# Performance work log

Hardware: AMD Instinct MI355X
Metric: run time of the kernel (lower is better)

## Reference

```python
import jax, jax.numpy as jnp
import numpy as np

GROUPS = 32
HEADS = 4
EPS_GN = 1e-5
EPS_DEN = 1e-6


def group_norm(x, gamma, beta):
    b, c, h, w = x.shape
    xg = x.reshape(b, GROUPS, (c // GROUPS) * h * w)
    mu = xg.mean(axis=-1, keepdims=True)
    var = xg.var(axis=-1, keepdims=True)
    xn = ((xg - mu) * jax.lax.rsqrt(var + EPS_GN)).reshape(b, c, h, w)
    return xn * gamma[None, :, None, None] + beta[None, :, None, None]


def setup_inputs() -> dict:
    key = jax.random.key(0)
    ks = jax.random.split(key, 4)
    b, c, h, w = 16, 256, 64, 64
    x = jax.random.normal(ks[0], (b, c, h, w), dtype=jnp.float32)
    gamma = jnp.ones((c,), jnp.float32)
    beta = jnp.zeros((c,), jnp.float32)
    w_qkv = jax.random.normal(ks[1], (3 * c, c), jnp.float32) * (1.0 / np.sqrt(c))
    b_qkv = jnp.zeros((3 * c,), jnp.float32)
    w_out = jax.random.normal(ks[2], (c, c), jnp.float32) * (1.0 / np.sqrt(c))
    b_out = jnp.zeros((c,), jnp.float32)
    return {"x": x, "gamma": gamma, "beta": beta, "w_qkv": w_qkv,
            "b_qkv": b_qkv, "w_out": w_out, "b_out": b_out}


def reference(x, gamma, beta, w_qkv, b_qkv, w_out, b_out):
    b, c, h, w = x.shape
    d = c // HEADS
    n = h * w
    xn = group_norm(x, gamma, beta)
    # 1x1 conv == channel GEMM: [b,3c,h,w]
    qkv = jnp.einsum('bchw,oc->bohw', xn, w_qkv) + b_qkv[None, :, None, None]
    q, k, v = jnp.split(qkv, 3, axis=1)
    # b (heads d) h w -> b heads d n
    q = q.reshape(b, HEADS, d, n)
    k = k.reshape(b, HEADS, d, n)
    v = v.reshape(b, HEADS, d, n)
    q = jax.nn.elu(q) + 1.0
    k = jax.nn.elu(k) + 1.0
    k_sum = k.sum(axis=-1)                                 # [b,H,d]
    kv = jnp.einsum('bhdn,bhen->bhde', k, v)               # [b,H,d,d]
    out = jnp.einsum('bhde,bhdn->bhen', kv, q)             # [b,H,d,n]
    denom = jnp.einsum('bhdn,bhd->bhn', q, k_sum)          # [b,H,n]
    out = out / (denom[:, :, None, :] + EPS_DEN)
    out = out.reshape(b, c, h, w)
    out = jnp.einsum('bchw,oc->bohw', out, w_out) + b_out[None, :, None, None]
    return out + x
```

## Files before the change

kernel.cpp:

```cpp
#include <hip/hip_runtime.h>
#include <stdint.h>

#define BATCH 16
#define CH    256
#define NSP   4096
#define NH    4
#define HD    64

typedef __attribute__((ext_vector_type(8))) short bf16x8;
typedef __attribute__((ext_vector_type(4))) float f32x4;
typedef __attribute__((ext_vector_type(4))) unsigned int u32x4;

__device__ __forceinline__ short f2bf(float f) {
    union { float f; unsigned u; } v; v.f = f;
    unsigned r = (v.u + 0x7fffu + ((v.u >> 16) & 1u)) >> 16;
    return (short)r;
}
__device__ __forceinline__ float bf2f(short s) {
    union { float f; unsigned u; } v; v.u = ((unsigned)(unsigned short)s) << 16;
    return v.f;
}

__global__ __launch_bounds__(256) void k_pre(
        const float* __restrict__ x, const float* __restrict__ wq, const float* __restrict__ wo,
        float* __restrict__ mu, float* __restrict__ rstd,
        short* __restrict__ wq_bf, short* __restrict__ wo_bf) {
    int bg = blockIdx.x;
    if (bg < 512) {
        const float4* p = (const float4*)(x + (size_t)bg * 32768);
        float s = 0.f, sq = 0.f;
        for (int i = threadIdx.x; i < 8192; i += 256) {
            float4 v = p[i];
            s  += v.x + v.y + v.z + v.w;
            sq += v.x * v.x + v.y * v.y + v.z * v.z + v.w * v.w;
        }
        for (int off = 32; off; off >>= 1) { s += __shfl_down(s, off); sq += __shfl_down(sq, off); }
        __shared__ float ls[4], lq[4];
        int w = threadIdx.x >> 6;
        if ((threadIdx.x & 63) == 0) { ls[w] = s; lq[w] = sq; }
        __syncthreads();
        if (threadIdx.x == 0) {
            float S = ls[0] + ls[1] + ls[2] + ls[3];
            float Q = lq[0] + lq[1] + lq[2] + lq[3];
            float m = S / 32768.f;
            float var = Q / 32768.f - m * m;
            mu[bg] = m; rstd[bg] = rsqrtf(var + 1e-5f);
        }
    } else {
        int idx = ((bg - 512) * 256 + threadIdx.x) * 4;
        float4 v;
        short* dst;
        if (idx < 196608) { v = *(const float4*)(wq + idx); dst = wq_bf + idx; }
        else              { v = *(const float4*)(wo + (idx - 196608)); dst = wo_bf + (idx - 196608); }
        unsigned p0 = ((unsigned)(unsigned short)f2bf(v.x)) | (((unsigned)(unsigned short)f2bf(v.y)) << 16);
        unsigned p1 = ((unsigned)(unsigned short)f2bf(v.z)) | (((unsigned)(unsigned short)f2bf(v.w)) << 16);
        uint2 pk; pk.x = p0; pk.y = p1;
        *(uint2*)dst = pk;
    }
}

__global__ __launch_bounds__(256) void k_gnqkv(
        const float* __restrict__ x, const float* __restrict__ gamma, const float* __restrict__ beta,
        const float* __restrict__ mu, const float* __restrict__ rstd,
        const short* __restrict__ wq_bf, const float* __restrict__ b_qkv,
        short* __restrict__ q_t, short* __restrict__ kvp_bf, float* __restrict__ ksp) {
    int b = blockIdx.y, nt = blockIdx.x;
    int n0 = nt * 64;
    __shared__ short Blds[64 * 264];
    __shared__ union UR {
        struct { short kst[64 * 72]; short vst[64 * 72]; } s;
        short cst[64 * 136];
    } R;
    int t = threadIdx.x, lane = t & 63, wv = t >> 6, lr = lane & 15, quad = lane >> 4;

    {
        const float* xb = x + (size_t)b * CH * NSP;
        int m = t & 15, cq = t >> 4;
        for (int cb = 0; cb < 16; cb++) {
            int c = cb * 16 + cq;
            int g = c >> 3;
            float sc = rstd[b * 32 + g] * gamma[c];
            float sh = beta[c] - mu[b * 32 + g] * sc;
            float4 v = *(const float4*)(xb + (size_t)c * NSP + n0 + m * 4);
            float vv[4] = {v.x, v.y, v.z, v.w};
            #pragma unroll
            for (int j = 0; j < 4; j++) {
                int n = m * 4 + j;
                int cc = c ^ (((n >> 4) & 3) << 3);
                Blds[n * 264 + cc] = f2bf(vv[j] * sc + sh);
            }
        }
    }
    __syncthreads();

    for (int h = 0; h < 4; h++) {
        int base_row = (wv < 2 ? 256 : 512) + h * 64;
        int sub = (wv & 1) * 32;
        f32x4 acc[2][4] = {};
        for (int k0 = 0; k0 < 256; k0 += 32) {
            bf16x8 afr[2], bfr[4];
            #pragma unroll
            for (int mi = 0; mi < 2; mi++)
                afr[mi] = *(const bf16x8*)(wq_bf + (size_t)(base_row + sub + mi * 16 + lr) * 256 + k0 + quad * 8);
            #pragma unroll
            for (int ni = 0; ni < 4; ni++) {
                int rr = ni * 16 + lr;
                bfr[ni] = *(const bf16x8*)(Blds + rr * 264 + ((k0 + quad * 8) ^ (((rr >> 4) & 3) << 3)));
            }
            #pragma unroll
            for (int mi = 0; mi < 2; mi++)
                #pragma unroll
                for (int ni = 0; ni < 4; ni++)
                    acc[mi][ni] = __builtin_amdgcn_mfma_f32_16x16x32_bf16(afr[mi], bfr[ni], acc[mi][ni], 0, 0, 0);
        }
        __syncthreads();
        short* dst = (wv < 2) ? R.s.kst : R.s.vst;
        bool is_k = (wv < 2);
        #pragma unroll
        for (int mi = 0; mi < 2; mi++)
          #pragma unroll
          for (int ni = 0; ni < 4; ni++)
            #pragma unroll
            for (int r = 0; r < 4; r++) {
                int ol = sub + mi * 16 + quad * 4 + r;
                int nl = ni * 16 + lr;
                float v = acc[mi][ni][r] + b_qkv[base_row + ol];
                if (is_k) v = v > 0.f ? v + 1.f : __expf(v);
                dst[ol * 72 + nl] = f2bf(v);
            }
        __syncthreads();
        {
            int d = t >> 2, nq = (t & 3) * 16;
            float s = 0.f;
            #pragma unroll
            for (int j = 0; j < 16; j++) s += bf2f(R.s.kst[d * 72 + nq + j]);
            s += __shfl_down(s, 2);
            s += __shfl_down(s, 1);
            if ((t & 3) == 0) ksp[((size_t)(b * 4 + h) * 64 + nt) * 64 + d] = s;
        }
        f32x4 acc2[4] = {};
        #pragma unroll
        for (int kk = 0; kk < 64; kk += 32) {
            bf16x8 af = *(const bf16x8*)(R.s.vst + (wv * 16 + lr) * 72 + kk + quad * 8);
            bf16x8 bfk[4];
            #pragma unroll
            for (int ni = 0; ni < 4; ni++)
                bfk[ni] = *(const bf16x8*)(R.s.kst + (ni * 16 + lr) * 72 + kk + quad * 8);
            #pragma unroll
            for (int ni = 0; ni < 4; ni++)
                acc2[ni] = __builtin_amdgcn_mfma_f32_16x16x32_bf16(af, bfk[ni], acc2[ni], 0, 0, 0);
        }
        short* kvdst = kvp_bf + ((size_t)(b * 4 + h) * 64 + nt) * 4096;
        #pragma unroll
        for (int ni = 0; ni < 4; ni++)
            #pragma unroll
            for (int r = 0; r < 4; r++)
                kvdst[(wv * 16 + quad * 4 + r) * 64 + ni * 16 + lr] = f2bf(acc2[ni][r]);
    }

    for (int mtq = 0; mtq < 2; mtq++) {
        f32x4 acc[2][4] = {};
        int wm = wv * 32;
        for (int k0 = 0; k0 < 256; k0 += 32) {
            bf16x8 afr[2], bfr[4];
            #pragma unroll
            for (int mi = 0; mi < 2; mi++)
                afr[mi] = *(const bf16x8*)(wq_bf + (size_t)(mtq * 128 + wm + mi * 16 + lr) * 256 + k0 + quad * 8);
            #pragma unroll
            for (int ni = 0; ni < 4; ni++) {
                int rr = ni * 16 + lr;
                bfr[ni] = *(const bf16x8*)(Blds + rr * 264 + ((k0 + quad * 8) ^ (((rr >> 4) & 3) << 3)));
            }
            #pragma unroll
            for (int mi = 0; mi < 2; mi++)
                #pragma unroll
                for (int ni = 0; ni < 4; ni++)
                    acc[mi][ni] = __builtin_amdgcn_mfma_f32_16x16x32_bf16(afr[mi], bfr[ni], acc[mi][ni], 0, 0, 0);
        }
        __syncthreads();
        #pragma unroll
        for (int mi = 0; mi < 2; mi++)
          #pragma unroll
          for (int ni = 0; ni < 4; ni++)
            #pragma unroll
            for (int r = 0; r < 4; r++) {
                int ol = wm + mi * 16 + quad * 4 + r;
                int nl = ni * 16 + lr;
                float v = acc[mi][ni][r] + b_qkv[mtq * 128 + ol];
                v = v > 0.f ? v + 1.f : __expf(v);
                R.cst[nl * 136 + ol] = f2bf(v);
            }
        __syncthreads();
        #pragma unroll
        for (int i = 0; i < 4; i++) {
            int ch = t + i * 256;
            int row = ch >> 4, o8 = (ch & 15) * 8;
            int hh = mtq * 2 + (o8 >> 6), d0 = o8 & 63;
            *(u32x4*)(q_t + ((size_t)(b * 4 + hh) * NSP + n0 + row) * HD + d0) =
                *(const u32x4*)(R.cst + row * 136 + o8);
        }
    }
}

__global__ __launch_bounds__(256) void k_kv_reduce(
        const short* __restrict__ kvp_bf, const float* __restrict__ ksp,
        short* __restrict__ kvT_bf, float* __restrict__ ksum_g) {
    int p = blockIdx.x, bh = blockIdx.y;
    int t = threadIdx.x;
    int chunk = p * 256 + t;
    const short* base = kvp_bf + (size_t)bh * 64 * 4096 + chunk * 8;
    float s[8] = {};
    for (int ntc = 0; ntc < 64; ntc++) {
        bf16x8 v = *(const bf16x8*)(base + (size_t)ntc * 4096);
        #pragma unroll
        for (int j = 0; j < 8; j++) s[j] += bf2f(v[j]);
    }
    bf16x8 rv;
    #pragma unroll
    for (int j = 0; j < 8; j++) rv[j] = f2bf(s[j]);
    *(bf16x8*)(kvT_bf + (size_t)bh * 4096 + chunk * 8) = rv;
    if (p == 0 && t < 64) {
        float ss = 0.f;
        for (int ntc = 0; ntc < 64; ntc++) ss += ksp[((size_t)bh * 64 + ntc) * 64 + t];
        ksum_g[bh * 64 + t] = ss;
    }
}

__global__ __launch_bounds__(256) void k_attn_out(
        const short* __restrict__ q_t, const short* __restrict__ kvT_bf,
        const float* __restrict__ ksum_g, const short* __restrict__ wo_bf,
        const float* __restrict__ b_out, const float* __restrict__ x,
        float* __restrict__ out) {
    int b = blockIdx.y, nt = blockIdx.x;
    int n0 = nt * 64;
    __shared__ short Battn[64 * 264];
    __shared__ short ql[64 * 72];
    __shared__ short kvl[64 * 72];
    __shared__ float ksl[64], dnl[64];
    int t = threadIdx.x, lane = t & 63, wv = t >> 6, lr = lane & 15, quad = lane >> 4;

    for (int h = 0; h < 4; h++) {
        int bh = b * 4 + h;
        #pragma unroll
        for (int i = 0; i < 2; i++) {
            int ch = t + i * 256;
            int row = ch >> 3, dc = (ch & 7) * 8;
            *(u32x4*)(ql + row * 72 + dc) =
                *(const u32x4*)(q_t + ((size_t)bh * NSP + n0 + row) * HD + dc);
            *(u32x4*)(kvl + row * 72 + dc) =
                *(const u32x4*)(kvT_bf + (size_t)bh * 4096 + row * 64 + dc);
        }
        if (t < 64) ksl[t] = ksum_g[bh * 64 + t];
        __syncthreads();
        if (t < 64) {
            float s = 0.f;
            #pragma unroll
            for (int d = 0; d < 64; d++) s += bf2f(ql[t * 72 + d]) * ksl[d];
            dnl[t] = 1.f / (s + 1e-6f);
        }
        __syncthreads();
        f32x4 acc[4] = {};
        #pragma unroll
        for (int kk = 0; kk < 64; kk += 32) {
            bf16x8 af = *(const bf16x8*)(ql + (wv * 16 + lr) * 72 + kk + quad * 8);
            bf16x8 bfr[4];
            #pragma unroll
            for (int ni = 0; ni < 4; ni++)
                bfr[ni] = *(const bf16x8*)(kvl + (ni * 16 + lr) * 72 + kk + quad * 8);
            #pragma unroll
            for (int ni = 0; ni < 4; ni++)
                acc[ni] = __builtin_amdgcn_mfma_f32_16x16x32_bf16(af, bfr[ni], acc[ni], 0, 0, 0);
        }
        float dn[4];
        #pragma unroll
        for (int r = 0; r < 4; r++) dn[r] = dnl[wv * 16 + quad * 4 + r];
        #pragma unroll
        for (int ni = 0; ni < 4; ni++)
            #pragma unroll
            for (int r = 0; r < 4; r++) {
                int n = wv * 16 + quad * 4 + r;
                Battn[n * 264 + h * 64 + ni * 16 + lr] = f2bf(acc[ni][r] * dn[r]);
            }
        __syncthreads();
    }

    for (int p = 0; p < 2; p++) {
        f32x4 acc[2][4] = {};
        int wm = wv * 32;
        for (int k0 = 0; k0 < 256; k0 += 32) {
            bf16x8 afr[2], bfr[4];
            #pragma unroll
            for (int mi = 0; mi < 2; mi++)
                afr[mi] = *(const bf16x8*)(wo_bf + (size_t)(p * 128 + wm + mi * 16 + lr) * 256 + k0 + quad * 8);
            #pragma unroll
            for (int ni = 0; ni < 4; ni++)
                bfr[ni] = *(const bf16x8*)(Battn + (ni * 16 + lr) * 264 + k0 + quad * 8);
            #pragma unroll
            for (int mi = 0; mi < 2; mi++)
                #pragma unroll
                for (int ni = 0; ni < 4; ni++)
                    acc[mi][ni] = __builtin_amdgcn_mfma_f32_16x16x32_bf16(afr[mi], bfr[ni], acc[mi][ni], 0, 0, 0);
        }
        #pragma unroll
        for (int mi = 0; mi < 2; mi++)
          #pragma unroll
          for (int ni = 0; ni < 4; ni++)
            #pragma unroll
            for (int r = 0; r < 4; r++) {
                int o = p * 128 + wm + mi * 16 + quad * 4 + r;
                int nl = ni * 16 + lr;
                size_t idx = ((size_t)b * CH + o) * NSP + n0 + nl;
                out[idx] = acc[mi][ni][r] + b_out[o] + x[idx];
            }
    }
}

extern "C" void kernel_launch(void* const* d_in, const int* in_sizes, int n_in,
                              void* d_out, int out_size, void* d_ws, size_t ws_size,
                              hipStream_t stream) {
    const float* x     = (const float*)d_in[0];
    const float* gamma = (const float*)d_in[1];
    const float* beta  = (const float*)d_in[2];
    const float* w_qkv = (const float*)d_in[3];
    const float* b_qkv = (const float*)d_in[4];
    const float* w_out = (const float*)d_in[5];
    const float* b_out = (const float*)d_in[6];
    float* out = (float*)d_out;

    char* ws = (char*)d_ws;
    size_t off = 0;
    float* mu     = (float*)(ws + off); off += 2048;
    float* rstd   = (float*)(ws + off); off += 2048;
    short* wq_bf  = (short*)(ws + off); off += (size_t)768 * 256 * 2;
    short* wo_bf  = (short*)(ws + off); off += (size_t)256 * 256 * 2;
    short* q_t    = (short*)(ws + off); off += (size_t)BATCH * NSP * CH * 2;
    short* kvp_bf = (short*)(ws + off); off += (size_t)64 * 64 * 4096 * 2;
    float* ksp    = (float*)(ws + off); off += (size_t)64 * 64 * 64 * 4;
    short* kvT_bf = (short*)(ws + off); off += (size_t)64 * 4096 * 2;
    float* ksum_g = (float*)(ws + off); off += (size_t)64 * 64 * 4;

    if (ws_size < off) return;

    k_pre<<<768, 256, 0, stream>>>(x, w_qkv, w_out, mu, rstd, wq_bf, wo_bf);
    k_gnqkv<<<dim3(64, 16), 256, 0, stream>>>(x, gamma, beta, mu, rstd, wq_bf, b_qkv, q_t, kvp_bf, ksp);
    k_kv_reduce<<<dim3(2, 64), 256, 0, stream>>>(kvp_bf, ksp, kvT_bf, ksum_g);
    k_attn_out<<<dim3(64, 16), 256, 0, stream>>>(q_t, kvT_bf, ksum_g, wo_bf, b_out, x, out);
}
```

Baseline: 258.4 us.

## Process two spatial tiles per block, preload weight fragments, split kv reduction

The GN+QKV and attention-output kernels now each handle two 64-column tiles per block, with half as many blocks. Weight A-fragments are loaded into registers for the whole K dimension before the MFMA loop. The attention kernel reads Q and kv straight from global memory instead of staging them in LDS, and it computes the denominators for all heads up front. The kv reduction kernel spreads the 64 partial sums across four wave groups with an LDS combine to get more parallelism. Together these aim to cut LDS traffic and load latency stalls, at the cost of higher register pressure and fewer blocks (512) to fill the CUs.

Measured after the change: 307.9 us. 19.1% more time.

```diff
diff --git a/kernel.cpp b/kernel.cpp
--- a/kernel.cpp
+++ b/kernel.cpp
@@ -64,8 +64,7 @@
         const float* __restrict__ mu, const float* __restrict__ rstd,
         const short* __restrict__ wq_bf, const float* __restrict__ b_qkv,
         short* __restrict__ q_t, short* __restrict__ kvp_bf, float* __restrict__ ksp) {
-    int b = blockIdx.y, nt = blockIdx.x;
-    int n0 = nt * 64;
+    int b = blockIdx.y;
     __shared__ short Blds[64 * 264];
     __shared__ union UR {
         struct { short kst[64 * 72]; short vst[64 * 72]; } s;
@@ -73,131 +72,147 @@
     } R;
     int t = threadIdx.x, lane = t & 63, wv = t >> 6, lr = lane & 15, quad = lane >> 4;
 
-    {
-        const float* xb = x + (size_t)b * CH * NSP;
-        int m = t & 15, cq = t >> 4;
-        for (int cb = 0; cb < 16; cb++) {
-            int c = cb * 16 + cq;
-            int g = c >> 3;
-            float sc = rstd[b * 32 + g] * gamma[c];
-            float sh = beta[c] - mu[b * 32 + g] * sc;
-            float4 v = *(const float4*)(xb + (size_t)c * NSP + n0 + m * 4);
-            float vv[4] = {v.x, v.y, v.z, v.w};
-            #pragma unroll
-            for (int j = 0; j < 4; j++) {
-                int n = m * 4 + j;
-                int cc = c ^ (((n >> 4) & 3) << 3);
-                Blds[n * 264 + cc] = f2bf(vv[j] * sc + sh);
-            }
-        }
-    }
-    __syncthreads();
-
-    for (int h = 0; h < 4; h++) {
-        int base_row = (wv < 2 ? 256 : 512) + h * 64;
-        int sub = (wv & 1) * 32;
-        f32x4 acc[2][4] = {};
-        for (int k0 = 0; k0 < 256; k0 += 32) {
-            bf16x8 afr[2], bfr[4];
+    for (int it = 0; it < 2; it++) {
+        int nt = blockIdx.x * 2 + it;
+        int n0 = nt * 64;
+
+        {
+            const float* xb = x + (size_t)b * CH * NSP;
+            int m = t & 15, cq = t >> 4;
+            #pragma unroll 4
+            for (int cb = 0; cb < 16; cb++) {
+                int c = cb * 16 + cq;
+                int g = c >> 3;
+                float sc = rstd[b * 32 + g] * gamma[c];
+                float sh = beta[c] - mu[b * 32 + g] * sc;
+                float4 v = *(const float4*)(xb + (size_t)c * NSP + n0 + m * 4);
+                float vv[4] = {v.x, v.y, v.z, v.w};
+                #pragma unroll
+                for (int j = 0; j < 4; j++) {
+                    int n = m * 4 + j;
+                    int cc = c ^ (((n >> 4) & 3) << 3);
+                    Blds[n * 264 + cc] = f2bf(vv[j] * sc + sh);
+                }
+            }
+        }
+        __syncthreads();
+
+        for (int h = 0; h < 4; h++) {
+            int br0 = (wv < 2 ? 256 : 512) + h * 64;
+            int sub = (wv & 1) * 32;
+            const short* wr = wq_bf + (size_t)(br0 + sub + lr) * 256 + quad * 8;
+            bf16x8 A0[8], A1[8];
+            #pragma unroll
+            for (int kk = 0; kk < 8; kk++) {
+                A0[kk] = *(const bf16x8*)(wr + kk * 32);
+                A1[kk] = *(const bf16x8*)(wr + 16 * 256 + kk * 32);
+            }
+            f32x4 acc[2][4] = {};
+            #pragma unroll
+            for (int kk = 0; kk < 8; kk++) {
+                bf16x8 bfr[4];
+                #pragma unroll
+                for (int ni = 0; ni < 4; ni++) {
+                    int rr = ni * 16 + lr;
+                    bfr[ni] = *(const bf16x8*)(Blds + rr * 264 + ((kk * 32 + quad * 8) ^ (((rr >> 4) & 3) << 3)));
+                }
+                #pragma unroll
+                for (int ni = 0; ni < 4; ni++) {
+                    acc[0][ni] = __builtin_amdgcn_mfma_f32_16x16x32_bf16(A0[kk], bfr[ni], acc[0][ni], 0, 0, 0);
+                    acc[1][ni] = __builtin_amdgcn_mfma_f32_16x16x32_bf16(A1[kk], bfr[ni], acc[1][ni], 0, 0, 0);
+                }
+            }
+            __syncthreads();
+            short* dst = (wv < 2) ? R.s.kst : R.s.vst;
+            bool is_k = (wv < 2);
             #pragma unroll
             for (int mi = 0; mi < 2; mi++)
-                afr[mi] = *(const bf16x8*)(wq_bf + (size_t)(base_row + sub + mi * 16 + lr) * 256 + k0 + quad * 8);
-            #pragma unroll
-            for (int ni = 0; ni < 4; ni++) {
-                int rr = ni * 16 + lr;
-                bfr[ni] = *(const bf16x8*)(Blds + rr * 264 + ((k0 + quad * 8) ^ (((rr >> 4) & 3) << 3)));
-            }
+              #pragma unroll
+              for (int ni = 0; ni < 4; ni++)
+                #pragma unroll
+                for (int r = 0; r < 4; r++) {
+                    int ol = sub + mi * 16 + quad * 4 + r;
+                    int nl = ni * 16 + lr;
+                    float v = acc[mi][ni][r] + b_qkv[br0 + ol];
+                    if (is_k) v = v > 0.f ? v + 1.f : __expf(v);
+                    dst[ol * 72 + nl] = f2bf(v);
+                }
+            __syncthreads();
+            {
+                int d = t >> 2, nq = (t & 3) * 16;
+                float s = 0.f;
+                #pragma unroll
+                for (int j = 0; j < 16; j++) s += bf2f(R.s.kst[d * 72 + nq + j]);
+                s += __shfl_down(s, 2);
+                s += __shfl_down(s, 1);
+                if ((t & 3) == 0) ksp[((size_t)(b * 4 + h) * 64 + nt) * 64 + d] = s;
+            }
+            f32x4 acc2[4] = {};
+            #pragma unroll
+            for (int kk = 0; kk < 64; kk += 32) {
+                bf16x8 af = *(const bf16x8*)(R.s.vst + (wv * 16 + lr) * 72 + kk + quad * 8);
+                bf16x8 bfk[4];
+                #pragma unroll
+                for (int ni = 0; ni < 4; ni++)
+                    bfk[ni] = *(const bf16x8*)(R.s.kst + (ni * 16 + lr) * 72 + kk + quad * 8);
+                #pragma unroll
+                for (int ni = 0; ni < 4; ni++)
+                    acc2[ni] = __builtin_amdgcn_mfma_f32_16x16x32_bf16(af, bfk[ni], acc2[ni], 0, 0, 0);
+            }
+            short* kvdst = kvp_bf + ((size_t)(b * 4 + h) * 64 + nt) * 4096;
+            #pragma unroll
+            for (int ni = 0; ni < 4; ni++)
+                #pragma unroll
+                for (int r = 0; r < 4; r++)
+                    kvdst[(wv * 16 + quad * 4 + r) * 64 + ni * 16 + lr] = f2bf(acc2[ni][r]);
+        }
+
+        for (int mtq = 0; mtq < 2; mtq++) {
+            int wm = wv * 32;
+            const short* wr = wq_bf + (size_t)(mtq * 128 + wm + lr) * 256 + quad * 8;
+            bf16x8 A0[8], A1[8];
+            #pragma unroll
+            for (int kk = 0; kk < 8; kk++) {
+                A0[kk] = *(const bf16x8*)(wr + kk * 32);
+                A1[kk] = *(const bf16x8*)(wr + 16 * 256 + kk * 32);
+            }
+            f32x4 acc[2][4] = {};
+            #pragma unroll
+            for (int kk = 0; kk < 8; kk++) {
+                bf16x8 bfr[4];
+                #pragma unroll
+                for (int ni = 0; ni < 4; ni++) {
+                    int rr = ni * 16 + lr;
+                    bfr[ni] = *(const bf16x8*)(Blds + rr * 264 + ((kk * 32 + quad * 8) ^ (((rr >> 4) & 3) << 3)));
+                }
+                #pragma unroll
+                for (int ni = 0; ni < 4; ni++) {
+                    acc[0][ni] = __builtin_amdgcn_mfma_f32_16x16x32_bf16(A0[kk], bfr[ni], acc[0][ni], 0, 0, 0);
+                    acc[1][ni] = __builtin_amdgcn_mfma_f32_16x16x32_bf16(A1[kk], bfr[ni], acc[1][ni], 0, 0, 0);
+                }
+            }
+            __syncthreads();
             #pragma unroll
             for (int mi = 0; mi < 2; mi++)
-                #pragma unroll
-                for (int ni = 0; ni < 4; ni++)
-                    acc[mi][ni] = __builtin_amdgcn_mfma_f32_16x16x32_bf16(afr[mi], bfr[ni], acc[mi][ni], 0, 0, 0);
-        }
-        __syncthreads();
-        short* dst = (wv < 2) ? R.s.kst : R.s.vst;
-        bool is_k = (wv < 2);
-        #pragma unroll
-        for (int mi = 0; mi < 2; mi++)
-          #pragma unroll
-          for (int ni = 0; ni < 4; ni++)
-            #pragma unroll
-            for (int r = 0; r < 4; r++) {
-                int ol = sub + mi * 16 + quad * 4 + r;
-                int nl = ni * 16 + lr;
-                float v = acc[mi][ni][r] + b_qkv[base_row + ol];
-                if (is_k) v = v > 0.f ? v + 1.f : __expf(v);
-                dst[ol * 72 + nl] = f2bf(v);
-            }
-        __syncthreads();
-        {
-            int d = t >> 2, nq = (t & 3) * 16;
-            float s = 0.f;
-            #pragma unroll
-            for (int j = 0; j < 16; j++) s += bf2f(R.s.kst[d * 72 + nq + j]);
-            s += __shfl_down(s, 2);
-            s += __shfl_down(s, 1);
-            if ((t & 3) == 0) ksp[((size_t)(b * 4 + h) * 64 + nt) * 64 + d] = s;
-        }
-        f32x4 acc2[4] = {};
-        #pragma unroll
-        for (int kk = 0; kk < 64; kk += 32) {
-            bf16x8 af = *(const bf16x8*)(R.s.vst + (wv * 16 + lr) * 72 + kk + quad * 8);
-            bf16x8 bfk[4];
-            #pragma unroll
-            for (int ni = 0; ni < 4; ni++)
-                bfk[ni] = *(const bf16x8*)(R.s.kst + (ni * 16 + lr) * 72 + kk + quad * 8);
-            #pragma unroll
-            for (int ni = 0; ni < 4; ni++)
-                acc2[ni] = __builtin_amdgcn_mfma_f32_16x16x32_bf16(af, bfk[ni], acc2[ni], 0, 0, 0);
-        }
-        short* kvdst = kvp_bf + ((size_t)(b * 4 + h) * 64 + nt) * 4096;
-        #pragma unroll
-        for (int ni = 0; ni < 4; ni++)
-            #pragma unroll
-            for (int r = 0; r < 4; r++)
-                kvdst[(wv * 16 + quad * 4 + r) * 64 + ni * 16 + lr] = f2bf(acc2[ni][r]);
-    }
-
-    for (int mtq = 0; mtq < 2; mtq++) {
-        f32x4 acc[2][4] = {};
-        int wm = wv * 32;
-        for (int k0 = 0; k0 < 256; k0 += 32) {
-            bf16x8 afr[2], bfr[4];
-            #pragma unroll
-            for (int mi = 0; mi < 2; mi++)
-                afr[mi] = *(const bf16x8*)(wq_bf + (size_t)(mtq * 128 + wm + mi * 16 + lr) * 256 + k0 + quad * 8);
-            #pragma unroll
-            for (int ni = 0; ni < 4; ni++) {
-                int rr = ni * 16 + lr;
-                bfr[ni] = *(const bf16x8*)(Blds + rr * 264 + ((k0 + quad * 8) ^ (((rr >> 4) & 3) << 3)));
-            }
-            #pragma unroll
-            for (int mi = 0; mi < 2; mi++)
-                #pragma unroll
-                for (int ni = 0; ni < 4; ni++)
-                    acc[mi][ni] = __builtin_amdgcn_mfma_f32_16x16x32_bf16(afr[mi], bfr[ni], acc[mi][ni], 0, 0, 0);
-        }
-        __syncthreads();
-        #pragma unroll
-        for (int mi = 0; mi < 2; mi++)
-          #pragma unroll
-          for (int ni = 0; ni < 4; ni++)
-            #pragma unroll
-            for (int r = 0; r < 4; r++) {
-                int ol = wm + mi * 16 + quad * 4 + r;
-                int nl = ni * 16 + lr;
-                float v = acc[mi][ni][r] + b_qkv[mtq * 128 + ol];
-                v = v > 0.f ? v + 1.f : __expf(v);
-                R.cst[nl * 136 + ol] = f2bf(v);
-            }
-        __syncthreads();
-        #pragma unroll
-        for (int i = 0; i < 4; i++) {
-            int ch = t + i * 256;
-            int row = ch >> 4, o8 = (ch & 15) * 8;
-            int hh = mtq * 2 + (o8 >> 6), d0 = o8 & 63;
-            *(u32x4*)(q_t + ((size_t)(b * 4 + hh) * NSP + n0 + row) * HD + d0) =
-                *(const u32x4*)(R.cst + row * 136 + o8);
+              #pragma unroll
+              for (int ni = 0; ni < 4; ni++)
+                #pragma unroll
+                for (int r = 0; r < 4; r++) {
+                    int ol = wm + mi * 16 + quad * 4 + r;
+                    int nl = ni * 16 + lr;
+                    float v = acc[mi][ni][r] + b_qkv[mtq * 128 + ol];
+                    v = v > 0.f ? v + 1.f : __expf(v);
+                    R.cst[nl * 136 + ol] = f2bf(v);
+                }
+            __syncthreads();
+            #pragma unroll
+            for (int i = 0; i < 4; i++) {
+                int ch = t + i * 256;
+                int row = ch >> 4, o8 = (ch & 15) * 8;
+                int hh = mtq * 2 + (o8 >> 6), d0 = o8 & 63;
+                *(u32x4*)(q_t + ((size_t)(b * 4 + hh) * NSP + n0 + row) * HD + d0) =
+                    *(const u32x4*)(R.cst + row * 136 + o8);
+            }
         }
     }
 }
@@ -206,23 +221,38 @@
         const short* __restrict__ kvp_bf, const float* __restrict__ ksp,
         short* __restrict__ kvT_bf, float* __restrict__ ksum_g) {
     int p = blockIdx.x, bh = blockIdx.y;
-    int t = threadIdx.x;
-    int chunk = p * 256 + t;
+    int t = threadIdx.x, lane = t & 63, grp = t >> 6;
+    int chunk = p * 64 + lane;
     const short* base = kvp_bf + (size_t)bh * 64 * 4096 + chunk * 8;
     float s[8] = {};
-    for (int ntc = 0; ntc < 64; ntc++) {
+    for (int ntc = grp * 16; ntc < grp * 16 + 16; ntc++) {
         bf16x8 v = *(const bf16x8*)(base + (size_t)ntc * 4096);
         #pragma unroll
         for (int j = 0; j < 8; j++) s[j] += bf2f(v[j]);
     }
-    bf16x8 rv;
-    #pragma unroll
-    for (int j = 0; j < 8; j++) rv[j] = f2bf(s[j]);
-    *(bf16x8*)(kvT_bf + (size_t)bh * 4096 + chunk * 8) = rv;
-    if (p == 0 && t < 64) {
+    __shared__ float red[4][64][8];
+    if (grp) {
+        #pragma unroll
+        for (int j = 0; j < 8; j++) red[grp][lane][j] = s[j];
+    }
+    __syncthreads();
+    if (grp == 0) {
+        bf16x8 rv;
+        #pragma unroll
+        for (int j = 0; j < 8; j++) {
+            float v = s[j] + red[1][lane][j] + red[2][lane][j] + red[3][lane][j];
+            rv[j] = f2bf(v);
+        }
+        *(bf16x8*)(kvT_bf + (size_t)bh * 4096 + chunk * 8) = rv;
+    }
+    if (p == 0) {
+        const float* kb = ksp + (size_t)bh * 64 * 64 + lane;
         float ss = 0.f;
-        for (int ntc = 0; ntc < 64; ntc++) ss += ksp[((size_t)bh * 64 + ntc) * 64 + t];
-        ksum_g[bh * 64 + t] = ss;
+        for (int ntc = grp * 16; ntc < grp * 16 + 16; ntc++) ss += kb[(size_t)ntc * 64];
+        __syncthreads();
+        red[grp][lane][0] = ss;
+        __syncthreads();
+        if (grp == 0) ksum_g[bh * 64 + lane] = ss + red[1][lane][0] + red[2][lane][0] + red[3][lane][0];
     }
 }
 
@@ -231,87 +261,91 @@
         const float* __restrict__ ksum_g, const short* __restrict__ wo_bf,
         const float* __restrict__ b_out, const float* __restrict__ x,
         float* __restrict__ out) {
-    int b = blockIdx.y, nt = blockIdx.x;
-    int n0 = nt * 64;
+    int b = blockIdx.y;
     __shared__ short Battn[64 * 264];
-    __shared__ short ql[64 * 72];
-    __shared__ short kvl[64 * 72];
-    __shared__ float ksl[64], dnl[64];
+    __shared__ float dnl[4][64];
     int t = threadIdx.x, lane = t & 63, wv = t >> 6, lr = lane & 15, quad = lane >> 4;
 
-    for (int h = 0; h < 4; h++) {
-        int bh = b * 4 + h;
-        #pragma unroll
-        for (int i = 0; i < 2; i++) {
-            int ch = t + i * 256;
-            int row = ch >> 3, dc = (ch & 7) * 8;
-            *(u32x4*)(ql + row * 72 + dc) =
-                *(const u32x4*)(q_t + ((size_t)bh * NSP + n0 + row) * HD + dc);
-            *(u32x4*)(kvl + row * 72 + dc) =
-                *(const u32x4*)(kvT_bf + (size_t)bh * 4096 + row * 64 + dc);
-        }
-        if (t < 64) ksl[t] = ksum_g[bh * 64 + t];
-        __syncthreads();
-        if (t < 64) {
+    for (int it = 0; it < 2; it++) {
+        int nt = blockIdx.x * 2 + it;
+        int n0 = nt * 64;
+
+        {
+            const short* qp = q_t + ((size_t)(b * 4 + wv) * NSP + n0 + lane) * HD;
+            const float* ks = ksum_g + (b * 4 + wv) * 64;
             float s = 0.f;
             #pragma unroll
-            for (int d = 0; d < 64; d++) s += bf2f(ql[t * 72 + d]) * ksl[d];
-            dnl[t] = 1.f / (s + 1e-6f);
-        }
-        __syncthreads();
-        f32x4 acc[4] = {};
-        #pragma unroll
-        for (int kk = 0; kk < 64; kk += 32) {
-            bf16x8 af = *(const bf16x8*)(ql + (wv * 16 + lr) * 72 + kk + quad * 8);
-            bf16x8 bfr[4];
+            for (int c8 = 0; c8 < 8; c8++) {
+                bf16x8 qv = *(const bf16x8*)(qp + c8 * 8);
+                #pragma unroll
+                for (int j = 0; j < 8; j++) s += bf2f(qv[j]) * ks[c8 * 8 + j];
+            }
+            dnl[wv][lane] = 1.f / (s + 1e-6f);
+        }
+        __syncthreads();
+
+        for (int h = 0; h < 4; h++) {
+            size_t bh = (size_t)(b * 4 + h);
+            const short* qbase = q_t + (bh * NSP + n0) * HD;
+            const short* kvbase = kvT_bf + bh * 4096;
+            bf16x8 af[2], bfr[2][4];
+            #pragma unroll
+            for (int kz = 0; kz < 2; kz++) {
+                af[kz] = *(const bf16x8*)(qbase + (wv * 16 + lr) * HD + kz * 32 + quad * 8);
+                #pragma unroll
+                for (int ni = 0; ni < 4; ni++)
+                    bfr[kz][ni] = *(const bf16x8*)(kvbase + (ni * 16 + lr) * HD + kz * 32 + quad * 8);
+            }
+            f32x4 acc[4] = {};
+            #pragma unroll
+            for (int kz = 0; kz < 2; kz++)
+                #pragma unroll
+                for (int ni = 0; ni < 4; ni++)
+                    acc[ni] = __builtin_amdgcn_mfma_f32_16x16x32_bf16(af[kz], bfr[kz][ni], acc[ni], 0, 0, 0);
             #pragma unroll
             for (int ni = 0; ni < 4; ni++)
-                bfr[ni] = *(const bf16x8*)(kvl + (ni * 16 + lr) * 72 + kk + quad * 8);
-            #pragma unroll
-            for (int ni = 0; ni < 4; ni++)
-                acc[ni] = __builtin_amdgcn_mfma_f32_16x16x32_bf16(af, bfr[ni], acc[ni], 0, 0, 0);
-        }
-        float dn[4];
-        #pragma unroll
-        for (int r = 0; r < 4; r++) dn[r] = dnl[wv * 16 + quad * 4 + r];
-        #pragma unroll
-        for (int ni = 0; ni < 4; ni++)
-            #pragma unroll
-            for (int r = 0; r < 4; r++) {
-                int n = wv * 16 + quad * 4 + r;
-                Battn[n * 264 + h * 64 + ni * 16 + lr] = f2bf(acc[ni][r] * dn[r]);
-            }
-        __syncthreads();
-    }
-
-    for (int p = 0; p < 2; p++) {
-        f32x4 acc[2][4] = {};
-        int wm = wv * 32;
-        for (int k0 = 0; k0 < 256; k0 += 32) {
-            bf16x8 afr[2], bfr[4];
+                #pragma unroll
+                for (int r = 0; r < 4; r++) {
+                    int n = wv * 16 + quad * 4 + r;
+                    Battn[n * 264 + h * 64 + ni * 16 + lr] = f2bf(acc[ni][r] * dnl[h][n]);
+                }
+        }
+        __syncthreads();
+
+        for (int p = 0; p < 2; p++) {
+            int rbase = p * 128 + wv * 32;
+            const short* wr = wo_bf + (size_t)(rbase + lr) * 256 + quad * 8;
+            bf16x8 A0[8], A1[8];
+            #pragma unroll
+            for (int kk = 0; kk < 8; kk++) {
+                A0[kk] = *(const bf16x8*)(wr + kk * 32);
+                A1[kk] = *(const bf16x8*)(wr + 16 * 256 + kk * 32);
+            }
+            f32x4 acc[2][4] = {};
+            #pragma unroll
+            for (int kk = 0; kk < 8; kk++) {
+                bf16x8 bfr[4];
+                #pragma unroll
+                for (int ni = 0; ni < 4; ni++)
+                    bfr[ni] = *(const bf16x8*)(Battn + (ni * 16 + lr) * 264 + kk * 32 + quad * 8);
+                #pragma unroll
+                for (int ni = 0; ni < 4; ni++) {
+                    acc[0][ni] = __builtin_amdgcn_mfma_f32_16x16x32_bf16(A0[kk], bfr[ni], acc[0][ni], 0, 0, 0);
+                    acc[1][ni] = __builtin_amdgcn_mfma_f32_16x16x32_bf16(A1[kk], bfr[ni], acc[1][ni], 0, 0, 0);
+                }
+            }
             #pragma unroll
             for (int mi = 0; mi < 2; mi++)
-                afr[mi] = *(const bf16x8*)(wo_bf + (size_t)(p * 128 + wm + mi * 16 + lr) * 256 + k0 + quad * 8);
-            #pragma unroll
-            for (int ni = 0; ni < 4; ni++)
-                bfr[ni] = *(const bf16x8*)(Battn + (ni * 16 + lr) * 264 + k0 + quad * 8);
-            #pragma unroll
-            for (int mi = 0; mi < 2; mi++)
-                #pragma unroll
-                for (int ni = 0; ni < 4; ni++)
-                    acc[mi][ni] = __builtin_amdgcn_mfma_f32_16x16x32_bf16(afr[mi], bfr[ni], acc[mi][ni], 0, 0, 0);
-        }
-        #pragma unroll
-        for (int mi = 0; mi < 2; mi++)
-          #pragma unroll
-          for (int ni = 0; ni < 4; ni++)
-            #pragma unroll
-            for (int r = 0; r < 4; r++) {
-                int o = p * 128 + wm + mi * 16 + quad * 4 + r;
-                int nl = ni * 16 + lr;
-                size_t idx = ((size_t)b * CH + o) * NSP + n0 + nl;
-                out[idx] = acc[mi][ni][r] + b_out[o] + x[idx];
-            }
+              #pragma unroll
+              for (int ni = 0; ni < 4; ni++)
+                #pragma unroll
+                for (int r = 0; r < 4; r++) {
+                    int o = rbase + mi * 16 + quad * 4 + r;
+                    int nl = ni * 16 + lr;
+                    size_t idx = ((size_t)b * CH + o) * NSP + n0 + nl;
+                    out[idx] = acc[mi][ni][r] + b_out[o] + x[idx];
+                }
+        }
     }
 }
 
@@ -342,7 +376,7 @@
     if (ws_size < off) return;
 
     k_pre<<<768, 256, 0, stream>>>(x, w_qkv, w_out, mu, rstd, wq_bf, wo_bf);
-    k_gnqkv<<<dim3(64, 16), 256, 0, stream>>>(x, gamma, beta, mu, rstd, wq_bf, b_qkv, q_t, kvp_bf, ksp);
-    k_kv_reduce<<<dim3(2, 64), 256, 0, stream>>>(kvp_bf, ksp, kvT_bf, ksum_g);
-    k_attn_out<<<dim3(64, 16), 256, 0, stream>>>(q_t, kvT_bf, ksum_g, wo_bf, b_out, x, out);
-}
+    k_gnqkv<<<dim3(32, 16), 256, 0, stream>>>(x, gamma, beta, mu, rstd, wq_bf, b_qkv, q_t, kvp_bf, ksp);
+    k_kv_reduce<<<dim3(8, 64), 256, 0, stream>>>(kvp_bf, ksp, kvT_bf, ksum_g);
+    k_attn_out<<<dim3(32, 16), 256, 0, stream>>>(q_t, kvT_bf, ksum_g, wo_bf, b_out, x, out);
+}
```
